# Performance work log

Hardware: AMD Instinct MI355X
Metric: run time of the kernel (lower is better)

The kernel has to match this reference:

```python
import jax, jax.numpy as jnp
import numpy as np

EMBED = 2048
MLP = 8192
EPS = 1e-5


def setup_inputs() -> dict:
    key = jax.random.key(0)
    ks = jax.random.split(key, 16)
    s = 0.02
    inp = {
        "x": jax.random.normal(ks[0], (2, 2048, EMBED), dtype=jnp.float32),
        "wq": jax.random.normal(ks[1], (EMBED, EMBED), dtype=jnp.float32) * s,
        "bq": jnp.zeros((EMBED,), jnp.float32),
        "wk": jax.random.normal(ks[2], (EMBED, EMBED), dtype=jnp.float32) * s,
        "bk": jnp.zeros((EMBED,), jnp.float32),
        "wv": jax.random.normal(ks[3], (EMBED, EMBED), dtype=jnp.float32) * s,
        "bv": jnp.zeros((EMBED,), jnp.float32),
        "wd": jax.random.normal(ks[4], (EMBED, EMBED), dtype=jnp.float32) * s,
        "bd": jnp.zeros((EMBED,), jnp.float32),
        "ln_g": jnp.ones((EMBED,), jnp.float32),
        "ln_b": jnp.zeros((EMBED,), jnp.float32),
        "w1": jax.random.normal(ks[5], (MLP, EMBED), dtype=jnp.float32) * s,
        "b1": jnp.zeros((MLP,), jnp.float32),
        "w2": jax.random.normal(ks[6], (EMBED, MLP), dtype=jnp.float32) * s,
        "b2": jnp.zeros((EMBED,), jnp.float32),
    }
    return inp


def _layernorm(x, g, b):
    mu = jnp.mean(x, axis=-1, keepdims=True)
    var = jnp.mean(jnp.square(x - mu), axis=-1, keepdims=True)
    return (x - mu) * jax.lax.rsqrt(var + EPS) * g + b


def reference(x, wq, bq, wk, bk, wv, bv, wd, bd, ln_g, ln_b, w1, b1, w2, b2):
    # Single-head attention; scale uses full embed_dim (rotary_emb.dim == embed_dim).
    q = jnp.einsum("bse,fe->bsf", x, wq) + bq
    k = jnp.einsum("bse,fe->bsf", x, wk) + bk
    v = jnp.einsum("bse,fe->bsf", x, wv) + bv
    scores = jnp.einsum("bqe,bke->bqk", q, k) / jnp.sqrt(jnp.float32(EMBED))
    probs = jax.nn.softmax(scores, axis=-1)
    ctx = jnp.einsum("bqk,bke->bqe", probs, v)
    attn_out = jnp.einsum("bse,fe->bsf", ctx, wd) + bd
    # residual (dropout is identity in eval mode)
    h = x + attn_out
    h = _layernorm(h, ln_g, ln_b)
    mlp = jnp.einsum("bse,fe->bsf", h, w1) + b1
    mlp = jax.nn.gelu(mlp, approximate=False)
    mlp = jnp.einsum("bsf,ef->bse", mlp, w2) + b2
    return h + mlp
```

## Files before the change

### kernel.cpp

```cpp
#include <hip/hip_runtime.h>
#include <math.h>


#define SEQ 2048
#define EMB 2048
#define MLPD 8192

typedef __attribute__((ext_vector_type(8))) short short8;
typedef __attribute__((ext_vector_type(4))) float floatx4;
typedef unsigned short ushort;

__device__ __forceinline__ short f2bf(float f) {
  union { float f; unsigned u; } v; v.f = f;
  unsigned r = v.u + 0x7FFFu + ((v.u >> 16) & 1u);
  return (short)(r >> 16);
}

__device__ __forceinline__ void gload16(const ushort* g, ushort* l) {
  __builtin_amdgcn_global_load_lds(
      (__attribute__((address_space(1))) void*)g,
      (__attribute__((address_space(3))) void*)(unsigned)(unsigned long)l,
      16, 0, 0);
}

enum { EPI_QKV = 0, EPI_SCORES = 1, EPI_PV = 2, EPI_RES = 3, EPI_GELU = 4 };

template<int EPI>
__global__ __launch_bounds__(512, 2)
void gemm256(const ushort* __restrict__ A, const ushort* __restrict__ B,
             const float* __restrict__ bias, void* __restrict__ Cp,
             int N, int K, int lda, int ldb, int ldc,
             long sA, long sB, long sC, float scale)
{
  extern __shared__ ushort lds[];
  const int t = threadIdx.x;
  const int lane = t & 63, w = t >> 6;
  const int wm = w >> 2, wn = w & 3;

  const int gx = gridDim.x, gy = gridDim.y;
  const int bid = blockIdx.y * gx + blockIdx.x;
  const int cpx = (gx * gy) >> 3;
  const int work = (bid & 7) * cpx + (bid >> 3);
  const long bm = (long)(work % gy) * 256;
  const long bn = (long)(work / gy) * 256;
  A += (long)blockIdx.z * sA;
  B += (long)blockIdx.z * sB;

  const int srow = (w << 3) + (lane >> 3);
  const int gcol = (lane & 7) ^ ((lane >> 3) & 7);
  const ushort* Ag = A + (bm + srow) * (long)lda + gcol * 8;
  const ushort* Bg = B + (bn + srow) * (long)ldb + gcol * 8;
  ushort* lw = lds + (w << 9);

#define STAGE(gb, ld, dst, kk) do {                         \
    const ushort* _g = (gb) + (kk);                         \
    gload16(_g, lw + (dst));                                \
    gload16(_g + 64L * (ld), lw + (dst) + 4096); } while (0)

  const int l15 = lane & 15, q = lane >> 4, swz = l15 & 7;
  const int kx0 = (q ^ swz) << 3;
  const int kx1 = ((4 + q) ^ swz) << 3;
  const int arow = (wm << 13) + l15 * 64;
  const int brow = 16384 + ((wn >> 1) << 13) + ((wn & 1) << 12) + l15 * 64;

  floatx4 acc[8][4];
#pragma unroll
  for (int m = 0; m < 8; ++m)
#pragma unroll
    for (int n = 0; n < 4; ++n) acc[m][n] = (floatx4)0.0f;

  const int NT = K >> 6;

  STAGE(Ag,              lda, 0,     0);
  STAGE(Ag + 128L * lda, lda, 8192,  0);
  STAGE(Bg,              ldb, 16384, 0);
  STAGE(Bg + 128L * ldb, ldb, 24576, 0);
  {
    const long k1p = (NT > 1) ? 64 : 0;
    STAGE(Bg,              ldb, 32768 + 16384, k1p);
    STAGE(Bg + 128L * ldb, ldb, 32768 + 24576, k1p);
  }
  asm volatile("s_waitcnt vmcnt(4)" ::: "memory");
  __builtin_amdgcn_s_barrier();

  for (int kt = 0; kt < NT; ++kt) {
    const int cur = (kt & 1) ? 32768 : 0;
    const int nxt = 32768 - cur;
    const long k1 = (long)((kt + 1 < NT) ? kt + 1 : NT - 1) << 6;
    const long k2 = (long)((kt + 2 < NT) ? kt + 2 : NT - 1) << 6;
    short8 a0[4], a1[4], b0[4], b1[4];

#pragma unroll
    for (int mf = 0; mf < 4; ++mf) {
      a0[mf] = *(const short8*)&lds[cur + arow + mf * 1024 + kx0];
      a1[mf] = *(const short8*)&lds[cur + arow + mf * 1024 + kx1];
    }
#pragma unroll
    for (int nf = 0; nf < 2; ++nf) {
      b0[nf] = *(const short8*)&lds[cur + brow + nf * 1024 + kx0];
      b1[nf] = *(const short8*)&lds[cur + brow + nf * 1024 + kx1];
    }
    STAGE(Ag, lda, nxt, k1);
    __builtin_amdgcn_s_barrier();
    asm volatile("s_waitcnt lgkmcnt(0)");
    __builtin_amdgcn_s_setprio(1);
#pragma unroll
    for (int mf = 0; mf < 4; ++mf)
#pragma unroll
      for (int nf = 0; nf < 2; ++nf) {
        acc[mf][nf] = __builtin_amdgcn_mfma_f32_16x16x32_bf16(a0[mf], b0[nf], acc[mf][nf], 0, 0, 0);
        acc[mf][nf] = __builtin_amdgcn_mfma_f32_16x16x32_bf16(a1[mf], b1[nf], acc[mf][nf], 0, 0, 0);
      }
    __builtin_amdgcn_s_setprio(0);
    __builtin_amdgcn_s_barrier();

#pragma unroll
    for (int nf = 2; nf < 4; ++nf) {
      b0[nf] = *(const short8*)&lds[cur + brow + nf * 1024 + kx0];
      b1[nf] = *(const short8*)&lds[cur + brow + nf * 1024 + kx1];
    }
    STAGE(Ag + 128L * lda, lda, nxt + 8192, k1);
    __builtin_amdgcn_s_barrier();
    asm volatile("s_waitcnt lgkmcnt(0)");
    __builtin_amdgcn_s_setprio(1);
#pragma unroll
    for (int mf = 0; mf < 4; ++mf)
#pragma unroll
      for (int nf = 2; nf < 4; ++nf) {
        acc[mf][nf] = __builtin_amdgcn_mfma_f32_16x16x32_bf16(a0[mf], b0[nf], acc[mf][nf], 0, 0, 0);
        acc[mf][nf] = __builtin_amdgcn_mfma_f32_16x16x32_bf16(a1[mf], b1[nf], acc[mf][nf], 0, 0, 0);
      }
    __builtin_amdgcn_s_setprio(0);
    __builtin_amdgcn_s_barrier();

#pragma unroll
    for (int mf = 0; mf < 4; ++mf) {
      a0[mf] = *(const short8*)&lds[cur + arow + (4 + mf) * 1024 + kx0];
      a1[mf] = *(const short8*)&lds[cur + arow + (4 + mf) * 1024 + kx1];
    }
    STAGE(Bg, ldb, cur + 16384, k2);
    __builtin_amdgcn_s_barrier();
    asm volatile("s_waitcnt lgkmcnt(0)");
    __builtin_amdgcn_s_setprio(1);
#pragma unroll
    for (int mf = 0; mf < 4; ++mf)
#pragma unroll
      for (int nf = 0; nf < 2; ++nf) {
        acc[4 + mf][nf] = __builtin_amdgcn_mfma_f32_16x16x32_bf16(a0[mf], b0[nf], acc[4 + mf][nf], 0, 0, 0);
        acc[4 + mf][nf] = __builtin_amdgcn_mfma_f32_16x16x32_bf16(a1[mf], b1[nf], acc[4 + mf][nf], 0, 0, 0);
      }
    __builtin_amdgcn_s_setprio(0);
    __builtin_amdgcn_s_barrier();

    STAGE(Bg + 128L * ldb, ldb, cur + 24576, k2);
    __builtin_amdgcn_s_setprio(1);
#pragma unroll
    for (int mf = 0; mf < 4; ++mf)
#pragma unroll
      for (int nf = 2; nf < 4; ++nf) {
        acc[4 + mf][nf] = __builtin_amdgcn_mfma_f32_16x16x32_bf16(a0[mf], b0[nf], acc[4 + mf][nf], 0, 0, 0);
        acc[4 + mf][nf] = __builtin_amdgcn_mfma_f32_16x16x32_bf16(a1[mf], b1[nf], acc[4 + mf][nf], 0, 0, 0);
      }
    __builtin_amdgcn_s_setprio(0);
    asm volatile("s_waitcnt vmcnt(4)" ::: "memory");
    __builtin_amdgcn_s_barrier();
  }
#undef STAGE

  const int lq = lane >> 4;
#pragma unroll
  for (int mf = 0; mf < 8; ++mf) {
#pragma unroll
    for (int nf = 0; nf < 4; ++nf) {
#pragma unroll
      for (int i = 0; i < 4; ++i) {
        const long r = bm + wm * 128 + mf * 16 + lq * 4 + i;
        const long c = bn + wn * 64 + nf * 16 + l15;
        float val = acc[mf][nf][i];
        if constexpr (EPI == EPI_QKV) {
          val += bias[c];
          ((ushort*)Cp)[r * (long)ldc + c] = (ushort)f2bf(val);
        } else if constexpr (EPI == EPI_SCORES) {
          ((float*)Cp)[(long)blockIdx.z * sC + r * (long)ldc + c] = val * scale;
        } else {
          val += bias[c];
          float g = 0.5f * val * (1.0f + erff(val * 0.70710678118f));
          ((ushort*)Cp)[r * (long)ldc + c] = (ushort)f2bf(g);
        }
      }
    }
  }
}

template<int EPI>
__global__ __launch_bounds__(256)
void gemm_bt(const ushort* __restrict__ A, const ushort* __restrict__ B,
             const float* __restrict__ bias, const float* __restrict__ res,
             void* __restrict__ Cp, int N, int K,
             int lda, int ldb, int ldc,
             long sA, long sB, long sC, float scale)
{
  __shared__ ushort As[128 * 32];
  __shared__ ushort Bs[128 * 32];

  const int t = threadIdx.x;
  const int lane = t & 63, wid = t >> 6;
  const int wm = wid >> 1, wn = wid & 1;
  const long bm = (long)blockIdx.y * 128;
  const long bn = (long)blockIdx.x * 128;
  A += (long)blockIdx.z * sA;
  B += (long)blockIdx.z * sB;

  const int srow = (wid << 5) + (lane >> 2);
  const int scol = (lane & 3) << 3;
  const ushort* a0 = A + (bm + srow) * (long)lda + scol;
  const ushort* a1 = a0 + 16L * lda;
  const ushort* b0 = B + (bn + srow) * (long)ldb + scol;
  const ushort* b1 = b0 + 16L * ldb;
  ushort* lA0 = As + (wid << 10);
  ushort* lA1 = lA0 + 512;
  ushort* lB0 = Bs + (wid << 10);
  ushort* lB1 = lB0 + 512;

  floatx4 acc[4][4];
#pragma unroll
  for (int m = 0; m < 4; ++m)
#pragma unroll
    for (int n = 0; n < 4; ++n) acc[m][n] = (floatx4)0.0f;

  const int l15 = lane & 15, kq = (lane >> 4) << 3;
  const int abase = ((wm << 6) + l15) * 32 + kq;
  const int bbase = ((wn << 6) + l15) * 32 + kq;

  for (int kb = 0; kb < K; kb += 32) {
    gload16(a0 + kb, lA0);
    gload16(a1 + kb, lA1);
    gload16(b0 + kb, lB0);
    gload16(b1 + kb, lB1);
    __syncthreads();

    short8 a[4], b[4];
#pragma unroll
    for (int m = 0; m < 4; ++m)
      a[m] = *reinterpret_cast<const short8*>(&As[abase + m * (16 * 32)]);
#pragma unroll
    for (int n = 0; n < 4; ++n)
      b[n] = *reinterpret_cast<const short8*>(&Bs[bbase + n * (16 * 32)]);
#pragma unroll
    for (int m = 0; m < 4; ++m)
#pragma unroll
      for (int n = 0; n < 4; ++n)
        acc[m][n] = __builtin_amdgcn_mfma_f32_16x16x32_bf16(a[m], b[n], acc[m][n], 0, 0, 0);
    __syncthreads();
  }

  const int lq = lane >> 4;
#pragma unroll
  for (int m = 0; m < 4; ++m) {
#pragma unroll
    for (int n = 0; n < 4; ++n) {
#pragma unroll
      for (int i = 0; i < 4; ++i) {
        const long r = bm + wm * 64 + m * 16 + lq * 4 + i;
        const long c = bn + wn * 64 + n * 16 + l15;
        float val = acc[m][n][i];
        if constexpr (EPI == EPI_SCORES) {
          ((float*)Cp)[(long)blockIdx.z * sC + r * (long)ldc + c] = val * scale;
        } else if constexpr (EPI == EPI_PV) {
          ((ushort*)Cp)[(long)blockIdx.z * sC + r * (long)ldc + c] = (ushort)f2bf(val);
        }
      }
    }
  }
}

__global__ __launch_bounds__(256)
void reduce2(const float* __restrict__ p0, const float* __restrict__ p1,
             const float* __restrict__ bias, const float* __restrict__ res,
             float* __restrict__ out)
{
  const long i = ((long)blockIdx.x * 256 + threadIdx.x) * 8;
  const int c = (int)(i & 2047);
  float4 a0 = *(const float4*)(p0 + i),  a1 = *(const float4*)(p0 + i + 4);
  float4 q0 = *(const float4*)(p1 + i),  q1 = *(const float4*)(p1 + i + 4);
  float4 r0 = *(const float4*)(res + i), r1 = *(const float4*)(res + i + 4);
  float4 b0 = *(const float4*)(bias + c), b1 = *(const float4*)(bias + c + 4);
  float4 o0 = {a0.x + q0.x + r0.x + b0.x, a0.y + q0.y + r0.y + b0.y,
               a0.z + q0.z + r0.z + b0.z, a0.w + q0.w + r0.w + b0.w};
  float4 o1 = {a1.x + q1.x + r1.x + b1.x, a1.y + q1.y + r1.y + b1.y,
               a1.z + q1.z + r1.z + b1.z, a1.w + q1.w + r1.w + b1.w};
  *(float4*)(out + i) = o0;
  *(float4*)(out + i + 4) = o1;
}

__global__ __launch_bounds__(256)
void cvt8(const float* __restrict__ s, ushort* __restrict__ d) {
  const long i = ((long)blockIdx.x * 256 + threadIdx.x) * 8;
  float4 a = *reinterpret_cast<const float4*>(s + i);
  float4 b = *reinterpret_cast<const float4*>(s + i + 4);
  short8 v;
  v[0] = f2bf(a.x); v[1] = f2bf(a.y); v[2] = f2bf(a.z); v[3] = f2bf(a.w);
  v[4] = f2bf(b.x); v[5] = f2bf(b.y); v[6] = f2bf(b.z); v[7] = f2bf(b.w);
  *reinterpret_cast<short8*>(d + i) = v;
}

__global__ __launch_bounds__(256)
void concat3(const float* __restrict__ b0, const float* __restrict__ b1,
             const float* __restrict__ b2, float* __restrict__ dst) {
  const int i = blockIdx.x * 256 + threadIdx.x;
  dst[i] = (i < 2048) ? b0[i] : (i < 4096) ? b1[i - 2048] : b2[i - 4096];
}

__global__ __launch_bounds__(256)
void transpose_v(const ushort* __restrict__ qkv, ushort* __restrict__ vT) {
  __shared__ ushort tile[32][33];
  const int b = blockIdx.z;
  const int s0 = blockIdx.x * 32, e0 = blockIdx.y * 32;
  const int tx = threadIdx.x & 31, ty = threadIdx.x >> 5;
#pragma unroll
  for (int i = 0; i < 4; ++i) {
    const long s = (long)b * SEQ + s0 + ty + i * 8;
    tile[ty + i * 8][tx] = qkv[s * 6144 + 4096 + e0 + tx];
  }
  __syncthreads();
#pragma unroll
  for (int i = 0; i < 4; ++i) {
    const long e = (long)b * SEQ + e0 + ty + i * 8;
    vT[e * SEQ + s0 + tx] = tile[tx][ty + i * 8];
  }
}

__global__ __launch_bounds__(256)
void softmax_rows(const float* __restrict__ S, ushort* __restrict__ P) {
  const long row = blockIdx.x;
  const float* src = S + row * 2048;
  const int t = threadIdx.x, lane = t & 63, wid = t >> 6;
  float4 a = *reinterpret_cast<const float4*>(src + t * 8);
  float4 b = *reinterpret_cast<const float4*>(src + t * 8 + 4);
  float v[8] = {a.x, a.y, a.z, a.w, b.x, b.y, b.z, b.w};
  float m = v[0];
#pragma unroll
  for (int i = 1; i < 8; ++i) m = fmaxf(m, v[i]);
#pragma unroll
  for (int o = 32; o; o >>= 1) m = fmaxf(m, __shfl_xor(m, o));
  __shared__ float rm[4], rs[4];
  if (!lane) rm[wid] = m;
  __syncthreads();
  m = fmaxf(fmaxf(rm[0], rm[1]), fmaxf(rm[2], rm[3]));
  float e[8], s = 0.f;
#pragma unroll
  for (int i = 0; i < 8; ++i) { e[i] = __expf(v[i] - m); s += e[i]; }
#pragma unroll
  for (int o = 32; o; o >>= 1) s += __shfl_xor(s, o);
  if (!lane) rs[wid] = s;
  __syncthreads();
  s = rs[0] + rs[1] + rs[2] + rs[3];
  const float inv = 1.0f / s;
  short8 wv;
#pragma unroll
  for (int i = 0; i < 8; ++i) wv[i] = f2bf(e[i] * inv);
  *reinterpret_cast<short8*>(P + row * 2048 + t * 8) = wv;
}

__global__ __launch_bounds__(256)
void layernorm_fused(const float* __restrict__ p0, const float* __restrict__ p1,
                     const float* __restrict__ bias, const float* __restrict__ res,
                     const float* __restrict__ g, const float* __restrict__ bb,
                     float* __restrict__ H, ushort* __restrict__ Hb) {
  const long row = blockIdx.x;
  const long base = row * 2048;
  const int t = threadIdx.x, lane = t & 63, wid = t >> 6;
  const long i = base + t * 8;
  const int c0 = t * 8;
  float v[8];
  {
    float4 a0 = *(const float4*)(p0 + i),  a1 = *(const float4*)(p0 + i + 4);
    float4 q0 = *(const float4*)(p1 + i),  q1 = *(const float4*)(p1 + i + 4);
    float4 r0 = *(const float4*)(res + i), r1 = *(const float4*)(res + i + 4);
    float4 b0 = *(const float4*)(bias + c0), b1 = *(const float4*)(bias + c0 + 4);
    v[0] = a0.x + q0.x + r0.x + b0.x; v[1] = a0.y + q0.y + r0.y + b0.y;
    v[2] = a0.z + q0.z + r0.z + b0.z; v[3] = a0.w + q0.w + r0.w + b0.w;
    v[4] = a1.x + q1.x + r1.x + b1.x; v[5] = a1.y + q1.y + r1.y + b1.y;
    v[6] = a1.z + q1.z + r1.z + b1.z; v[7] = a1.w + q1.w + r1.w + b1.w;
  }
  float s = 0.f, ss = 0.f;
#pragma unroll
  for (int i2 = 0; i2 < 8; ++i2) { s += v[i2]; ss += v[i2] * v[i2]; }
#pragma unroll
  for (int o = 32; o; o >>= 1) { s += __shfl_xor(s, o); ss += __shfl_xor(ss, o); }
  __shared__ float r1s[4], r2s[4];
  if (!lane) { r1s[wid] = s; r2s[wid] = ss; }
  __syncthreads();
  s = r1s[0] + r1s[1] + r1s[2] + r1s[3];
  ss = r2s[0] + r2s[1] + r2s[2] + r2s[3];
  const float mu = s * (1.0f / 2048.0f);
  const float var = ss * (1.0f / 2048.0f) - mu * mu;
  const float inv = rsqrtf(var + 1e-5f);
  float o0[8];
  short8 wv;
#pragma unroll
  for (int i2 = 0; i2 < 8; ++i2) {
    const int c = c0 + i2;
    o0[i2] = (v[i2] - mu) * inv * g[c] + bb[c];
    wv[i2] = f2bf(o0[i2]);
  }
  float4 w0 = {o0[0], o0[1], o0[2], o0[3]}, w1 = {o0[4], o0[5], o0[6], o0[7]};
  *reinterpret_cast<float4*>(H + i) = w0;
  *reinterpret_cast<float4*>(H + i + 4) = w1;
  *reinterpret_cast<short8*>(Hb + i) = wv;
}

extern "C" void kernel_launch(void* const* d_in, const int* in_sizes, int n_in,
                              void* d_out, int out_size, void* d_ws, size_t ws_size,
                              hipStream_t stream) {
  const float* x    = (const float*)d_in[0];
  const float* wq   = (const float*)d_in[1];
  const float* bq   = (const float*)d_in[2];
  const float* wk   = (const float*)d_in[3];
  const float* bk   = (const float*)d_in[4];
  const float* wv   = (const float*)d_in[5];
  const float* bv   = (const float*)d_in[6];
  const float* wd   = (const float*)d_in[7];
  const float* bd   = (const float*)d_in[8];
  const float* ln_g = (const float*)d_in[9];
  const float* ln_b = (const float*)d_in[10];
  const float* w1   = (const float*)d_in[11];
  const float* b1   = (const float*)d_in[12];
  const float* w2   = (const float*)d_in[13];
  const float* b2   = (const float*)d_in[14];
  float* out = (float*)d_out;

  (void)hipFuncSetAttribute((const void*)&gemm256<EPI_QKV>,
      hipFuncAttributeMaxDynamicSharedMemorySize, 131072);
  (void)hipFuncSetAttribute((const void*)&gemm256<EPI_GELU>,
      hipFuncAttributeMaxDynamicSharedMemorySize, 131072);
  (void)hipFuncSetAttribute((const void*)&gemm256<EPI_SCORES>,
      hipFuncAttributeMaxDynamicSharedMemorySize, 131072);

  char* p = (char*)d_ws;
  const size_t MB = 1048576;
  ushort* wdb    = (ushort*)(p + 0 * MB);
  ushort* w1b    = (ushort*)(p + 8 * MB);
  ushort* w2b    = (ushort*)(p + 40 * MB);
  float*  bqkv   = (float*) (p + 72 * MB);
  ushort* xb     = (ushort*)(p + 73 * MB);
  ushort* probs  = xb;
  ushort* qkv    = (ushort*)(p + 89 * MB);
  float*  partA  = (float*) (p + 89 * MB);
  ushort* mlpb   = (ushort*)(p + 89 * MB);
  ushort* vT     = (ushort*)(p + 137 * MB);
  ushort* wqkvb  = (ushort*)(p + 153 * MB);
  float*  scores = (float*) (p + 153 * MB);
  ushort* ctx    = (ushort*)(p + 153 * MB);
  float*  partM0 = (float*) (p + 0 * MB);
  float*  partM1 = (float*) (p + 153 * MB);
  float*  h      = (float*) (p + 185 * MB);
  ushort* hb     = (ushort*)(p + 217 * MB);

  const dim3 blk(256), blk512(512);
  const long SQ = (long)SEQ * SEQ;

  cvt8<<<4096, blk, 0, stream>>>(x, xb);
  cvt8<<<2048, blk, 0, stream>>>(wq, wqkvb);
  cvt8<<<2048, blk, 0, stream>>>(wk, wqkvb + 4194304);
  cvt8<<<2048, blk, 0, stream>>>(wv, wqkvb + 8388608);
  cvt8<<<2048, blk, 0, stream>>>(wd, wdb);
  cvt8<<<8192, blk, 0, stream>>>(w1, w1b);
  cvt8<<<8192, blk, 0, stream>>>(w2, w2b);
  concat3<<<24, blk, 0, stream>>>(bq, bk, bv, bqkv);

  gemm256<EPI_QKV><<<dim3(24, 16, 1), blk512, 131072, stream>>>(
      xb, wqkvb, bqkv, qkv, 6144, 2048, 2048, 2048, 6144, 0, 0, 0, 1.f);

  transpose_v<<<dim3(64, 64, 2), blk, 0, stream>>>(qkv, vT);

  gemm_bt<EPI_SCORES><<<dim3(16, 16, 2), blk, 0, stream>>>(
      qkv, qkv + 2048, nullptr, nullptr, scores, 2048, 2048, 6144, 6144, 2048,
      2048L * 6144, 2048L * 6144, SQ, 0.022097086912079608f);

  softmax_rows<<<dim3(4096), blk, 0, stream>>>(scores, probs);

  gemm_bt<EPI_PV><<<dim3(16, 16, 2), blk, 0, stream>>>(
      probs, vT, nullptr, nullptr, ctx, 2048, 2048, 2048, 2048, 2048,
      SQ, SQ, SQ, 1.f);

  gemm256<EPI_SCORES><<<dim3(8, 16, 2), blk512, 131072, stream>>>(
      ctx, wdb, nullptr, partA, 2048, 1024, 2048, 2048, 2048,
      1024, 1024, 8388608, 1.f);

  layernorm_fused<<<4096, blk, 0, stream>>>(
      partA, partA + 8388608, bd, x, ln_g, ln_b, h, hb);

  gemm256<EPI_GELU><<<dim3(32, 16, 1), blk512, 131072, stream>>>(
      hb, w1b, b1, mlpb, 8192, 2048, 2048, 2048, 8192, 0, 0, 0, 1.f);

  gemm256<EPI_SCORES><<<dim3(8, 16, 2), blk512, 131072, stream>>>(
      mlpb, w2b, nullptr, partM0, 2048, 4096, 8192, 8192, 2048,
      4096, 4096, (long)(153 * MB / 4), 1.f);
  reduce2<<<4096, blk, 0, stream>>>(partM0, partM1, b2, h, out);
}
```

Measured before the change: 673.0 us.

## Restructure GEMM main loop into 2x unrolled ping-pong with register-prefetched fragments

Rewrites the 256x256 bf16 GEMM k-loop so LDS fragment reads for the next sub-block are issued before the current MFMA block. Each loop iteration now handles two k-tiles with fixed double-buffer offsets, and both A and B are prefetched two tiles ahead with a wait of vmcnt(8)/vmcnt(4). The intent is to hide LDS latency behind MFMAs and cut index arithmetic. It also removes the XCD-aware block remapping in favour of plain blockIdx tiling, which may hurt L2 locality across chiplets. The unrolled loop assumes NT is even, and more fragment registers are live at once, which raises VGPR pressure.

```diff
diff --git a/kernel.cpp b/kernel.cpp
--- a/kernel.cpp
+++ b/kernel.cpp
@@ -36,32 +36,32 @@
   const int t = threadIdx.x;
   const int lane = t & 63, w = t >> 6;
   const int wm = w >> 2, wn = w & 3;
-
-  const int gx = gridDim.x, gy = gridDim.y;
-  const int bid = blockIdx.y * gx + blockIdx.x;
-  const int cpx = (gx * gy) >> 3;
-  const int work = (bid & 7) * cpx + (bid >> 3);
-  const long bm = (long)(work % gy) * 256;
-  const long bn = (long)(work / gy) * 256;
+  const long bm = (long)blockIdx.y * 256;
+  const long bn = (long)blockIdx.x * 256;
   A += (long)blockIdx.z * sA;
   B += (long)blockIdx.z * sB;
 
   const int srow = (w << 3) + (lane >> 3);
   const int gcol = (lane & 7) ^ ((lane >> 3) & 7);
-  const ushort* Ag = A + (bm + srow) * (long)lda + gcol * 8;
-  const ushort* Bg = B + (bn + srow) * (long)ldb + gcol * 8;
+  const ushort* pA0  = A + (bm + srow) * (long)lda + gcol * 8;
+  const ushort* pA0b = pA0 + 64L * lda;
+  const ushort* pA1  = pA0 + 128L * lda;
+  const ushort* pA1b = pA0 + 192L * lda;
+  const ushort* pB0  = B + (bn + srow) * (long)ldb + gcol * 8;
+  const ushort* pB0b = pB0 + 64L * ldb;
+  const ushort* pB1  = pB0 + 128L * ldb;
+  const ushort* pB1b = pB0 + 192L * ldb;
   ushort* lw = lds + (w << 9);
-
-#define STAGE(gb, ld, dst, kk) do {                         \
-    const ushort* _g = (gb) + (kk);                         \
-    gload16(_g, lw + (dst));                                \
-    gload16(_g + 64L * (ld), lw + (dst) + 4096); } while (0)
 
   const int l15 = lane & 15, q = lane >> 4, swz = l15 & 7;
   const int kx0 = (q ^ swz) << 3;
   const int kx1 = ((4 + q) ^ swz) << 3;
   const int arow = (wm << 13) + l15 * 64;
   const int brow = 16384 + ((wn >> 1) << 13) + ((wn & 1) << 12) + l15 * 64;
+  const int rA0_0 = arow + kx0,     rA1_0 = arow + kx1;
+  const int rB0_0 = brow + kx0,     rB1_0 = brow + kx1;
+  const int rA0_1 = rA0_0 + 32768,  rA1_1 = rA1_0 + 32768;
+  const int rB0_1 = rB0_0 + 32768,  rB1_1 = rB1_0 + 32768;
 
   floatx4 acc[8][4];
 #pragma unroll
@@ -69,103 +69,84 @@
 #pragma unroll
     for (int n = 0; n < 4; ++n) acc[m][n] = (floatx4)0.0f;
 
+  short8 al[4], al2[4], ah[4], ah2[4], bl[2], bl2[2], bh[2], bh2[2];
+
+#define GL(P, LOFF, KO) gload16((P) + (KO), lw + (LOFF))
+#define STG(P, PB, LOFF, KO) do { GL(P, LOFF, KO); GL(PB, (LOFF) + 4096, KO); } while (0)
+#define LDS8(IDX) (*(const short8*)&lds[IDX])
+#define LGKM0 asm volatile("s_waitcnt lgkmcnt(0)" ::: "memory")
+#define BARR() __builtin_amdgcn_s_barrier()
+
+#define RD_AL(RA, RA2) do { _Pragma("unroll") for (int mf = 0; mf < 4; ++mf) { \
+    al[mf]  = LDS8((RA)  + mf * 1024); al2[mf] = LDS8((RA2) + mf * 1024); } } while (0)
+#define RD_AH(RA, RA2) do { _Pragma("unroll") for (int mf = 0; mf < 4; ++mf) { \
+    ah[mf]  = LDS8((RA)  + (4 + mf) * 1024); ah2[mf] = LDS8((RA2) + (4 + mf) * 1024); } } while (0)
+#define RD_BL(RB, RB2) do { _Pragma("unroll") for (int nf = 0; nf < 2; ++nf) { \
+    bl[nf]  = LDS8((RB)  + nf * 1024); bl2[nf] = LDS8((RB2) + nf * 1024); } } while (0)
+#define RD_BH(RB, RB2) do { _Pragma("unroll") for (int nf = 0; nf < 2; ++nf) { \
+    bh[nf]  = LDS8((RB)  + (2 + nf) * 1024); bh2[nf] = LDS8((RB2) + (2 + nf) * 1024); } } while (0)
+
+#define MM(MO, NO, AX, AX2, BX, BX2) do {                                     \
+    __builtin_amdgcn_s_setprio(1);                                            \
+    _Pragma("unroll") for (int mf = 0; mf < 4; ++mf)                          \
+      _Pragma("unroll") for (int nf = 0; nf < 2; ++nf) {                      \
+        acc[(MO)+mf][(NO)+nf] = __builtin_amdgcn_mfma_f32_16x16x32_bf16(      \
+            AX[mf], BX[nf], acc[(MO)+mf][(NO)+nf], 0, 0, 0);                  \
+        acc[(MO)+mf][(NO)+nf] = __builtin_amdgcn_mfma_f32_16x16x32_bf16(      \
+            AX2[mf], BX2[nf], acc[(MO)+mf][(NO)+nf], 0, 0, 0);                \
+      }                                                                       \
+    __builtin_amdgcn_s_setprio(0);                                            \
+  } while (0)
+
+#define KTILE(CUR, RA0c, RA1c, RB0c, RB1c, RA0n, RA1n, RB0n, RB1n, KO) do {   \
+                                                                     \
+    RD_BH(RB0c, RB1c);                                                        \
+    MM(0, 0, al, al2, bl, bl2);                                               \
+    LGKM0; BARR();                                                            \
+                                                                     \
+    RD_AH(RA0c, RA1c);                                                        \
+    STG(pB0, pB0b, (CUR) + 16384, KO);                                        \
+    STG(pB1, pB1b, (CUR) + 24576, KO);                                        \
+    MM(0, 2, al, al2, bh, bh2);                                               \
+    asm volatile("s_waitcnt vmcnt(4)" ::: "memory");                          \
+    LGKM0; BARR();                                                            \
+                                                                     \
+    RD_AL(RA0n, RA1n);                                                        \
+    STG(pA0, pA0b, (CUR) + 0, KO);                                            \
+    MM(4, 0, ah, ah2, bl, bl2);                                               \
+    LGKM0; BARR();                                                            \
+                                                                     \
+    RD_BL(RB0n, RB1n);                                                        \
+    STG(pA1, pA1b, (CUR) + 8192, KO);                                         \
+    MM(4, 2, ah, ah2, bh, bh2);                                               \
+    LGKM0; BARR();                                                            \
+  } while (0)
+
+  STG(pB0, pB0b, 16384, 0);          STG(pB1, pB1b, 24576, 0);
+  STG(pA0, pA0b, 0, 0);              STG(pA1, pA1b, 8192, 0);
+  STG(pB0, pB0b, 32768 + 16384, 64); STG(pB1, pB1b, 32768 + 24576, 64);
+  STG(pA0, pA0b, 32768 + 0, 64);     STG(pA1, pA1b, 32768 + 8192, 64);
+  asm volatile("s_waitcnt vmcnt(8)" ::: "memory");
+  BARR();
+  RD_AL(rA0_0, rA1_0);
+  RD_BL(rB0_0, rB1_0);
+  LGKM0; BARR();
+
   const int NT = K >> 6;
-
-  STAGE(Ag,              lda, 0,     0);
-  STAGE(Ag + 128L * lda, lda, 8192,  0);
-  STAGE(Bg,              ldb, 16384, 0);
-  STAGE(Bg + 128L * ldb, ldb, 24576, 0);
-  {
-    const long k1p = (NT > 1) ? 64 : 0;
-    STAGE(Bg,              ldb, 32768 + 16384, k1p);
-    STAGE(Bg + 128L * ldb, ldb, 32768 + 24576, k1p);
-  }
-  asm volatile("s_waitcnt vmcnt(4)" ::: "memory");
-  __builtin_amdgcn_s_barrier();
-
-  for (int kt = 0; kt < NT; ++kt) {
-    const int cur = (kt & 1) ? 32768 : 0;
-    const int nxt = 32768 - cur;
-    const long k1 = (long)((kt + 1 < NT) ? kt + 1 : NT - 1) << 6;
-    const long k2 = (long)((kt + 2 < NT) ? kt + 2 : NT - 1) << 6;
-    short8 a0[4], a1[4], b0[4], b1[4];
-
-#pragma unroll
-    for (int mf = 0; mf < 4; ++mf) {
-      a0[mf] = *(const short8*)&lds[cur + arow + mf * 1024 + kx0];
-      a1[mf] = *(const short8*)&lds[cur + arow + mf * 1024 + kx1];
-    }
-#pragma unroll
-    for (int nf = 0; nf < 2; ++nf) {
-      b0[nf] = *(const short8*)&lds[cur + brow + nf * 1024 + kx0];
-      b1[nf] = *(const short8*)&lds[cur + brow + nf * 1024 + kx1];
-    }
-    STAGE(Ag, lda, nxt, k1);
-    __builtin_amdgcn_s_barrier();
-    asm volatile("s_waitcnt lgkmcnt(0)");
-    __builtin_amdgcn_s_setprio(1);
-#pragma unroll
-    for (int mf = 0; mf < 4; ++mf)
-#pragma unroll
-      for (int nf = 0; nf < 2; ++nf) {
-        acc[mf][nf] = __builtin_amdgcn_mfma_f32_16x16x32_bf16(a0[mf], b0[nf], acc[mf][nf], 0, 0, 0);
-        acc[mf][nf] = __builtin_amdgcn_mfma_f32_16x16x32_bf16(a1[mf], b1[nf], acc[mf][nf], 0, 0, 0);
-      }
-    __builtin_amdgcn_s_setprio(0);
-    __builtin_amdgcn_s_barrier();
-
-#pragma unroll
-    for (int nf = 2; nf < 4; ++nf) {
-      b0[nf] = *(const short8*)&lds[cur + brow + nf * 1024 + kx0];
-      b1[nf] = *(const short8*)&lds[cur + brow + nf * 1024 + kx1];
-    }
-    STAGE(Ag + 128L * lda, lda, nxt + 8192, k1);
-    __builtin_amdgcn_s_barrier();
-    asm volatile("s_waitcnt lgkmcnt(0)");
-    __builtin_amdgcn_s_setprio(1);
-#pragma unroll
-    for (int mf = 0; mf < 4; ++mf)
-#pragma unroll
-      for (int nf = 2; nf < 4; ++nf) {
-        acc[mf][nf] = __builtin_amdgcn_mfma_f32_16x16x32_bf16(a0[mf], b0[nf], acc[mf][nf], 0, 0, 0);
-        acc[mf][nf] = __builtin_amdgcn_mfma_f32_16x16x32_bf16(a1[mf], b1[nf], acc[mf][nf], 0, 0, 0);
-      }
-    __builtin_amdgcn_s_setprio(0);
-    __builtin_amdgcn_s_barrier();
-
-#pragma unroll
-    for (int mf = 0; mf < 4; ++mf) {
-      a0[mf] = *(const short8*)&lds[cur + arow + (4 + mf) * 1024 + kx0];
-      a1[mf] = *(const short8*)&lds[cur + arow + (4 + mf) * 1024 + kx1];
-    }
-    STAGE(Bg, ldb, cur + 16384, k2);
-    __builtin_amdgcn_s_barrier();
-    asm volatile("s_waitcnt lgkmcnt(0)");
-    __builtin_amdgcn_s_setprio(1);
-#pragma unroll
-    for (int mf = 0; mf < 4; ++mf)
-#pragma unroll
-      for (int nf = 0; nf < 2; ++nf) {
-        acc[4 + mf][nf] = __builtin_amdgcn_mfma_f32_16x16x32_bf16(a0[mf], b0[nf], acc[4 + mf][nf], 0, 0, 0);
-        acc[4 + mf][nf] = __builtin_amdgcn_mfma_f32_16x16x32_bf16(a1[mf], b1[nf], acc[4 + mf][nf], 0, 0, 0);
-      }
-    __builtin_amdgcn_s_setprio(0);
-    __builtin_amdgcn_s_barrier();
-
-    STAGE(Bg + 128L * ldb, ldb, cur + 24576, k2);
-    __builtin_amdgcn_s_setprio(1);
-#pragma unroll
-    for (int mf = 0; mf < 4; ++mf)
-#pragma unroll
-      for (int nf = 2; nf < 4; ++nf) {
-        acc[4 + mf][nf] = __builtin_amdgcn_mfma_f32_16x16x32_bf16(a0[mf], b0[nf], acc[4 + mf][nf], 0, 0, 0);
-        acc[4 + mf][nf] = __builtin_amdgcn_mfma_f32_16x16x32_bf16(a1[mf], b1[nf], acc[4 + mf][nf], 0, 0, 0);
-      }
-    __builtin_amdgcn_s_setprio(0);
-    asm volatile("s_waitcnt vmcnt(4)" ::: "memory");
-    __builtin_amdgcn_s_barrier();
-  }
-#undef STAGE
+  for (int kt = 0; kt < NT; kt += 2) {
+    const int k2 = ((kt + 2 < NT) ? kt + 2 : NT - 1) << 6;
+    const int k3 = ((kt + 3 < NT) ? kt + 3 : NT - 1) << 6;
+    KTILE(0,     rA0_0, rA1_0, rB0_0, rB1_0, rA0_1, rA1_1, rB0_1, rB1_1, k2);
+    KTILE(32768, rA0_1, rA1_1, rB0_1, rB1_1, rA0_0, rA1_0, rB0_0, rB1_0, k3);
+  }
+#undef KTILE
+#undef MM
+#undef RD_AL
+#undef RD_AH
+#undef RD_BL
+#undef RD_BH
+#undef STG
+#undef GL
 
   const int lq = lane >> 4;
 #pragma unroll
```

Result: slower. 733.0 us (+8.9%).
